# Kernel optimization log

Hardware: AMD Instinct MI355X
Metric: run time of the kernel (lower is better)

## Reference

```python
import jax, jax.numpy as jnp
import numpy as np

M_GRAPHS = 16384
L_FRAGS = 64
L_NODES = 512
N_FOCAL = 3 * M_GRAPHS
N_NEXT = 4 * M_GRAPHS
N_PARTIAL = 262144
D = 64  # Z_dim = EGNN_layer_dim = fragment_library_dim = MLP hidden dim


def _mlp(x, W1, b1, W2, b2):
    # EGNN_MLP: Linear -> LeakyReLU(0.01) -> Linear
    return jnp.dot(jax.nn.leaky_relu(jnp.dot(x, W1) + b1), W2) + b2


def _segment_softmax(scores, seg, num_segments):
    m = jax.ops.segment_max(scores, seg, num_segments=num_segments)
    e = jnp.exp(scores - m[seg])
    s = jax.ops.segment_sum(e, seg, num_segments=num_segments)
    return e / s[seg]


def setup_inputs() -> dict:
    key = jax.random.key(0)
    ks = jax.random.split(key, 32)
    f32 = jnp.float32
    inp = {
        'fragment_library_features': jax.random.normal(ks[0], (L_FRAGS, D), f32),
        'fragment_library_node_features': jax.random.normal(ks[1], (L_NODES, D), f32),
        'graph_subgraph_focal_features_concat': jax.random.normal(ks[2], (M_GRAPHS, D), f32),
        'h_partial': jax.random.normal(ks[3], (N_PARTIAL, D), f32),
        'h_focal': jax.random.normal(ks[4], (N_FOCAL, D), f32),
        'next_atom_type_library_idx': jax.random.randint(ks[5], (M_GRAPHS,), 0, L_FRAGS),
        'stop_mask': jnp.ones((M_GRAPHS,), jnp.bool_),
        'stop_focal_mask': jnp.ones((N_FOCAL,), jnp.bool_),
        'masked_focal_batch_index_reindexed': jnp.arange(N_FOCAL) % M_GRAPHS,
        'focal_attachment_index_rel_partial': jax.random.randint(ks[6], (M_GRAPHS,), 0, N_PARTIAL),
        'next_atom_attachment_indices': jax.random.randint(ks[7], (N_NEXT,), 0, L_NODES),
        'masked_next_atom_attachment_batch_index_reindexed': jnp.arange(N_NEXT) % M_GRAPHS,
        'masked_multihot_next_attachments': jnp.ones((N_NEXT,), jnp.bool_),
    }
    def lin(k, din, dout):
        return jax.random.normal(k, (din, dout), f32) * (1.0 / np.sqrt(din))
    dims = {'stop': (D, 1), 'fatt': (2 * D, 1), 'nfrag': (3 * D, 1), 'nfatt': (4 * D, 1), 'bond': (4 * D, 4)}
    i = 8
    for name, (din, dout) in dims.items():
        inp[name + '_W1'] = lin(ks[i], din, D)
        inp[name + '_b1'] = jax.random.normal(ks[i + 1], (D,), f32) * 0.01
        inp[name + '_W2'] = lin(ks[i + 2], D, dout)
        inp[name + '_b2'] = jax.random.normal(ks[i + 3], (dout,), f32) * 0.01
        i += 4
    return inp


def _forward(flf, flnf, gsf, h_partial, h_focal,
             next_atom_type_library_idx, stop_idx, focal_idx,
             masked_focal_seg, focal_att_idx_rel_partial,
             next_atom_att_idx, next_att_seg, mh_idx,
             stop_W1, stop_b1, stop_W2, stop_b2,
             fatt_W1, fatt_b1, fatt_W2, fatt_b2,
             nfrag_W1, nfrag_b1, nfrag_W2, nfrag_b2,
             nfatt_W1, nfatt_b1, nfatt_W2, nfatt_b2,
             bond_W1, bond_b1, bond_W2, bond_b2):
    # stop scores over all (graph, subgraph, focal) rows
    stop_logits = _mlp(gsf, stop_W1, stop_b1, stop_W2, stop_b2)  # [B, 1]

    h_focal_masked = h_focal[focal_idx]                          # [Nf, D]
    gsf_masked = gsf[stop_idx]                                   # [M, D]
    M = gsf_masked.shape[0]

    # focal attachment scoring: gather graph feats per focal candidate, concat, MLP, segment softmax
    x_fatt = jnp.concatenate([gsf_masked[masked_focal_seg], h_focal_masked], axis=1)  # [Nf, 2D]
    fatt_scores = _mlp(x_fatt, fatt_W1, fatt_b1, fatt_W2, fatt_b2)[:, 0]
    fatt_softmax = _segment_softmax(fatt_scores, masked_focal_seg, M)                 # [Nf]

    # focal atom features gathered from partial-graph node embeddings
    focal_atom_feats = h_partial[focal_att_idx_rel_partial[stop_idx]]                 # [M, D]
    g_focalAtom = jnp.concatenate([gsf_masked, focal_atom_feats], axis=1)             # [M, 2D]

    # cross-product scoring vs fragment library; concat-then-linear == split matmul (no [M,L,3D] materialization)
    din = g_focalAtom.shape[1]
    hA = jnp.dot(g_focalAtom, nfrag_W1[:din])                                         # [M, H]
    hB = jnp.dot(flf, nfrag_W1[din:])                                                 # [L, H]
    hidden = jax.nn.leaky_relu(hA[:, None, :] + hB[None, :, :] + nfrag_b1)            # [M, L, H]
    next_atom_fragment_logits = (jnp.einsum('mlh,ho->mlo', hidden, nfrag_W2) + nfrag_b2)[:, :, 0]  # [M, L]

    # chosen next-fragment features
    next_frag_feats = flf[next_atom_type_library_idx[stop_idx]]                       # [M, D]
    g_nextFrag = jnp.concatenate([g_focalAtom, next_frag_feats], axis=1)              # [M, 3D]

    # next-fragment attachment scoring over candidate library nodes
    next_att_feats = flnf[next_atom_att_idx]                                          # [Nn, D]
    x_nfatt = jnp.concatenate([g_nextFrag[next_att_seg], next_att_feats], axis=1)     # [Nn, 4D]
    nfatt_scores = _mlp(x_nfatt, nfatt_W1, nfatt_b1, nfatt_W2, nfatt_b2)[:, 0]
    nfatt_softmax = _segment_softmax(nfatt_scores, next_att_seg, M)                   # [Nn]

    # bond typing: scatter_mean of equivalent next-atom features per graph
    eq_feats = flnf[next_atom_att_idx[mh_idx]]                                        # [Ne, D]
    seg_mh = next_att_seg[mh_idx]
    sums = jax.ops.segment_sum(eq_feats, seg_mh, num_segments=M)
    cnt = jax.ops.segment_sum(jnp.ones(seg_mh.shape[0], eq_feats.dtype), seg_mh, num_segments=M)
    pooled = sums / jnp.maximum(cnt, 1.0)[:, None]                                    # [M, D]
    g_bond = jnp.concatenate([g_nextFrag, pooled], axis=1)                            # [M, 4D]
    bond_types_logits = _mlp(g_bond, bond_W1, bond_b1, bond_W2, bond_b2)              # [M, 4]

    return (stop_logits, next_atom_fragment_logits, fatt_softmax, nfatt_softmax, bond_types_logits)


def reference(fragment_library_features, fragment_library_node_features,
              graph_subgraph_focal_features_concat, h_partial, h_focal,
              next_atom_type_library_idx, stop_mask, stop_focal_mask,
              masked_focal_batch_index_reindexed, focal_attachment_index_rel_partial,
              next_atom_attachment_indices, masked_next_atom_attachment_batch_index_reindexed,
              masked_multihot_next_attachments,
              stop_W1, stop_b1, stop_W2, stop_b2,
              fatt_W1, fatt_b1, fatt_W2, fatt_b2,
              nfrag_W1, nfrag_b1, nfrag_W2, nfrag_b2,
              nfatt_W1, nfatt_b1, nfatt_W2, nfatt_b2,
              bond_W1, bond_b1, bond_W2, bond_b2):
    # masks are concrete -> convert boolean masks to static index arrays
    stop_idx = np.nonzero(np.asarray(stop_mask))[0]
    focal_idx = np.nonzero(np.asarray(stop_focal_mask))[0]
    mh_idx = np.nonzero(np.asarray(masked_multihot_next_attachments))[0]
    return _forward(fragment_library_features, fragment_library_node_features,
                    graph_subgraph_focal_features_concat, h_partial, h_focal,
                    next_atom_type_library_idx, stop_idx, focal_idx,
                    masked_focal_batch_index_reindexed, focal_attachment_index_rel_partial,
                    next_atom_attachment_indices, masked_next_atom_attachment_batch_index_reindexed,
                    mh_idx,
                    stop_W1, stop_b1, stop_W2, stop_b2,
                    fatt_W1, fatt_b1, fatt_W2, fatt_b2,
                    nfrag_W1, nfrag_b1, nfrag_W2, nfrag_b2,
                    nfatt_W1, nfatt_b1, nfatt_W2, nfatt_b2,
                    bond_W1, bond_b1, bond_W2, bond_b2)
```

## Files before the change

### kernel.cpp

```cpp
#include <hip/hip_runtime.h>
#include <math.h>

#define MG 16384
#define NFOC (3 * MG)
#define NNXT (4 * MG)

typedef float f32x4 __attribute__((ext_vector_type(4)));
typedef short s16x8 __attribute__((ext_vector_type(8)));

#define WT_STOP 0
#define WT_FATT 4096
#define WT_NFRAG 12288
#define WT_NFATT 20480
#define WT_BOND 36864
#define WT_TOTAL 53248

#define SW(r, b) ((b) ^ (((r) & 7) << 4))


__device__ __forceinline__ float lrelu(float x) { return x > 0.f ? x : 0.01f * x; }

__device__ __forceinline__ unsigned short f2bf(float f) {
  union { float f; unsigned u; } a;
  a.f = f;
  unsigned u = a.u;
  unsigned r = (u + 0x7fffu + ((u >> 16) & 1u)) >> 16;
  return (unsigned short)r;
}

__global__ void prep(const float* __restrict__ flf,
                     const float* __restrict__ stopW1,
                     const float* __restrict__ fattW1,
                     const float* __restrict__ nfragW1,
                     const float* __restrict__ nfattW1,
                     const float* __restrict__ bondW1,
                     float* __restrict__ hB4, unsigned short* __restrict__ wt) {
  int b = blockIdx.x, t = threadIdx.x;
  if (b < 16) {
    int l = b * 4 + (t >> 6), h = t & 63;
    float acc = 0.f;
#pragma unroll 8
    for (int k = 0; k < 64; ++k)
      acc = fmaf(flf[l * 64 + k], nfragW1[(128 + k) * 64 + h], acc);
    hB4[(h >> 2) * 256 + l * 4 + (h & 3)] = acc;
  } else {
    int e = (b - 16) * 256 + t;
    if (e < WT_TOTAL) {
      int k_all = e >> 6, col = e & 63;
      const float* src;
      int k, base;
      if (k_all < 64) { src = stopW1; k = k_all; base = WT_STOP; }
      else if (k_all < 192) { src = fattW1; k = k_all - 64; base = WT_FATT; }
      else if (k_all < 320) { src = nfragW1; k = k_all - 192; base = WT_NFRAG; }
      else if (k_all < 576) { src = nfattW1; k = k_all - 320; base = WT_NFATT; }
      else { src = bondW1; k = k_all - 576; base = WT_BOND; }
      int kt = k >> 5, kg = (k >> 3) & 3, ki = k & 7;
      wt[base + (((kt * 4 + kg) * 64 + col) << 3) + ki] = f2bf(src[k * 64 + col]);
    }
  }
}

__device__ __forceinline__ float4 stage_row(char* tileBase, int r, int c4,
                                            const float* srcRow) {
  float4 v = *((const float4*)srcRow + c4);
  unsigned long long pk =
      (unsigned long long)f2bf(v.x) | ((unsigned long long)f2bf(v.y) << 16) |
      ((unsigned long long)f2bf(v.z) << 32) | ((unsigned long long)f2bf(v.w) << 48);
  *(unsigned long long*)(tileBase + r * 128 + SW(r, c4 * 8)) = pk;
  return v;
}

__device__ __forceinline__ s16x8 ldA(const char* tile, int ktLocal, int lane) {
  int r = lane & 15, kg = lane >> 4;
  int b = ktLocal * 64 + kg * 16;
  return *(const s16x8*)(tile + r * 128 + SW(r, b));
}

__device__ __forceinline__ s16x8 ldB(const unsigned short* wt, int base,
                                     int ktGlobal, int kg, int col) {
  return *(const s16x8*)(wt + base + (((ktGlobal * 4 + kg) * 64 + col) << 3));
}

__global__ __launch_bounds__(256, 8) void decoder_main(
    const float* __restrict__ flf, const float* __restrict__ flnf,
    const float* __restrict__ gsf, const float* __restrict__ hpart,
    const float* __restrict__ hfoc,
    const int* __restrict__ nidx, const int* __restrict__ faidx,
    const int* __restrict__ naidx,
    const float* __restrict__ stopB1, const float* __restrict__ stopW2,
    const float* __restrict__ stopB2,
    const float* __restrict__ fattB1, const float* __restrict__ fattW2,
    const float* __restrict__ fattB2,
    const float* __restrict__ nfragB1, const float* __restrict__ nfragW2,
    const float* __restrict__ nfragB2,
    const float* __restrict__ nfattB1, const float* __restrict__ nfattW2,
    const float* __restrict__ nfattB2,
    const float* __restrict__ bondB1, const float* __restrict__ bondW2,
    const float* __restrict__ bondB2,
    const float* __restrict__ hB4, const unsigned short* __restrict__ wt,
    float* __restrict__ out) {
  const int tid = threadIdx.x;
  const int lane = tid & 63;
  const int w = tid >> 6;
  const int kg = lane >> 4;
  const int cl = lane & 15;
  const int col = w * 16 + cl;
  const int bid = (int)blockIdx.x;
  const int type = bid >> 10;
  const int m0 = (bid & 1023) * 16;

  float* o_stop = out;
  float* o_nfrag = out + MG;
  float* o_fatt = out + MG + MG * 64;
  float* o_nfatt = o_fatt + NFOC;
  float* o_bond = o_nfatt + NNXT;

  __shared__ char tiles[14336];
  __shared__ float hAl[16][68];
  __shared__ float scp[4][4][16];
  char* TG = tiles;
  char* TP = tiles + 2048;
  char* T2 = tiles + 4096;
  char* T3 = tiles + 6144;

  {
    int r = tid >> 4, c4 = tid & 15;
    int m = m0 + r;
    stage_row(TG, r, c4, gsf + (size_t)m * 64);
    stage_row(TP, r, c4, hpart + (size_t)faidx[m] * 64);
    if (type == 0) {
#pragma unroll
      for (int rr = 0; rr < 3; ++rr)
        stage_row(T2 + rr * 2048, r, c4, hfoc + (size_t)(m + rr * MG) * 64);
    } else if (type == 1) {
      stage_row(T2, r, c4, flf + (size_t)nidx[m] * 64);
#pragma unroll
      for (int rr = 0; rr < 4; ++rr)
        stage_row(T3 + rr * 2048, r, c4, flnf + (size_t)naidx[m + rr * MG] * 64);
    } else {
      stage_row(T2, r, c4, flf + (size_t)nidx[m] * 64);
      float px = 0.f, py = 0.f, pz = 0.f, pw = 0.f;
#pragma unroll
      for (int rr = 0; rr < 4; ++rr) {
        float4 v = *((const float4*)(flnf + (size_t)naidx[m + rr * MG] * 64) + c4);
        px += v.x; py += v.y; pz += v.z; pw += v.w;
      }
      unsigned long long pk = (unsigned long long)f2bf(0.25f * px) |
                              ((unsigned long long)f2bf(0.25f * py) << 16) |
                              ((unsigned long long)f2bf(0.25f * pz) << 32) |
                              ((unsigned long long)f2bf(0.25f * pw) << 48);
      *(unsigned long long*)(T3 + r * 128 + SW(r, c4 * 8)) = pk;
    }
  }
  __syncthreads();

#define MFMA(a, b, c) __builtin_amdgcn_mfma_f32_16x16x32_bf16(a, b, c, 0, 0, 0)
#define RED16(p, slot)                                                     \
  {                                                                        \
    _Pragma("unroll") for (int off = 1; off < 16; off <<= 1) {             \
      p[0] += __shfl_xor(p[0], off); p[1] += __shfl_xor(p[1], off);        \
      p[2] += __shfl_xor(p[2], off); p[3] += __shfl_xor(p[3], off);        \
    }                                                                      \
    if (cl == 0) {                                                         \
      float* d = &scp[w][slot][kg * 4];                                    \
      d[0] = p[0]; d[1] = p[1]; d[2] = p[2]; d[3] = p[3];                  \
    }                                                                      \
  }

  if (type == 0) {
    {
      float b1 = stopB1[col];
      f32x4 acc = {b1, b1, b1, b1};
      acc = MFMA(ldA(TG, 0, lane), ldB(wt, WT_STOP, 0, kg, col), acc);
      acc = MFMA(ldA(TG, 1, lane), ldB(wt, WT_STOP, 1, kg, col), acc);
      float w2 = stopW2[col];
      f32x4 p;
#pragma unroll
      for (int i = 0; i < 4; ++i) p[i] = lrelu(acc[i]) * w2;
      RED16(p, 0);
    }
    {
      float b1 = fattB1[col];
      f32x4 aS = {b1, b1, b1, b1};
      aS = MFMA(ldA(TG, 0, lane), ldB(wt, WT_FATT, 0, kg, col), aS);
      aS = MFMA(ldA(TG, 1, lane), ldB(wt, WT_FATT, 1, kg, col), aS);
      float w2 = fattW2[col];
#pragma unroll
      for (int rr = 0; rr < 3; ++rr) {
        f32x4 acc = aS;
        acc = MFMA(ldA(T2 + rr * 2048, 0, lane), ldB(wt, WT_FATT, 2, kg, col), acc);
        acc = MFMA(ldA(T2 + rr * 2048, 1, lane), ldB(wt, WT_FATT, 3, kg, col), acc);
        f32x4 p;
#pragma unroll
        for (int i = 0; i < 4; ++i) p[i] = lrelu(acc[i]) * w2;
        RED16(p, 1 + rr);
      }
    }
    {
      float b1 = nfragB1[col];
      f32x4 acc = {b1, b1, b1, b1};
      acc = MFMA(ldA(TG, 0, lane), ldB(wt, WT_NFRAG, 0, kg, col), acc);
      acc = MFMA(ldA(TG, 1, lane), ldB(wt, WT_NFRAG, 1, kg, col), acc);
      acc = MFMA(ldA(TP, 0, lane), ldB(wt, WT_NFRAG, 2, kg, col), acc);
      acc = MFMA(ldA(TP, 1, lane), ldB(wt, WT_NFRAG, 3, kg, col), acc);
#pragma unroll
      for (int i = 0; i < 4; ++i) hAl[kg * 4 + i][col] = acc[i];
    }
    __syncthreads();
    {
      float accL[4] = {0.f, 0.f, 0.f, 0.f};
#pragma unroll
      for (int hg = 0; hg < 16; ++hg) {
        f32x4 hb = *(const f32x4*)(hB4 + hg * 256 + lane * 4);
        f32x4 w2v = *(const f32x4*)(nfragW2 + hg * 4);
#pragma unroll
        for (int mi = 0; mi < 4; ++mi) {
          f32x4 ha = *(const f32x4*)(&hAl[w * 4 + mi][hg * 4]);
#pragma unroll
          for (int j = 0; j < 4; ++j) {
            float x = ha[j] + hb[j];
            accL[mi] = fmaf(fmaxf(x, 0.01f * x), w2v[j], accL[mi]);
          }
        }
      }
#pragma unroll
      for (int mi = 0; mi < 4; ++mi)
        o_nfrag[(size_t)(m0 + w * 4 + mi) * 64 + lane] = accL[mi] + nfragB2[0];
    }
    if (tid < 32) {
      int mm = tid & 15;
      int m = m0 + mm;
      if (tid < 16) {
        float s = scp[0][0][mm] + scp[1][0][mm] + scp[2][0][mm] + scp[3][0][mm];
        o_stop[m] = s + stopB2[0];
      } else {
        float sc[3];
#pragma unroll
        for (int r = 0; r < 3; ++r)
          sc[r] = scp[0][1 + r][mm] + scp[1][1 + r][mm] + scp[2][1 + r][mm] +
                  scp[3][1 + r][mm] + fattB2[0];
        float mx = fmaxf(fmaxf(sc[0], sc[1]), sc[2]);
        float e0 = expf(sc[0] - mx), e1 = expf(sc[1] - mx), e2 = expf(sc[2] - mx);
        float inv = 1.f / (e0 + e1 + e2);
        o_fatt[m] = e0 * inv;
        o_fatt[m + MG] = e1 * inv;
        o_fatt[m + 2 * MG] = e2 * inv;
      }
    }
  } else if (type == 1) {
    {
      float b1 = nfattB1[col];
      f32x4 aS = {b1, b1, b1, b1};
      aS = MFMA(ldA(TG, 0, lane), ldB(wt, WT_NFATT, 0, kg, col), aS);
      aS = MFMA(ldA(TG, 1, lane), ldB(wt, WT_NFATT, 1, kg, col), aS);
      aS = MFMA(ldA(TP, 0, lane), ldB(wt, WT_NFATT, 2, kg, col), aS);
      aS = MFMA(ldA(TP, 1, lane), ldB(wt, WT_NFATT, 3, kg, col), aS);
      aS = MFMA(ldA(T2, 0, lane), ldB(wt, WT_NFATT, 4, kg, col), aS);
      aS = MFMA(ldA(T2, 1, lane), ldB(wt, WT_NFATT, 5, kg, col), aS);
      float w2 = nfattW2[col];
#pragma unroll
      for (int rr = 0; rr < 4; ++rr) {
        f32x4 acc = aS;
        acc = MFMA(ldA(T3 + rr * 2048, 0, lane), ldB(wt, WT_NFATT, 6, kg, col), acc);
        acc = MFMA(ldA(T3 + rr * 2048, 1, lane), ldB(wt, WT_NFATT, 7, kg, col), acc);
        f32x4 p;
#pragma unroll
        for (int i = 0; i < 4; ++i) p[i] = lrelu(acc[i]) * w2;
        RED16(p, rr);
      }
    }
    __syncthreads();
    if (tid < 16) {
      int m = m0 + tid;
      float sc[4];
#pragma unroll
      for (int r = 0; r < 4; ++r)
        sc[r] = scp[0][r][tid] + scp[1][r][tid] + scp[2][r][tid] +
                scp[3][r][tid] + nfattB2[0];
      float mx = fmaxf(fmaxf(sc[0], sc[1]), fmaxf(sc[2], sc[3]));
      float e0 = expf(sc[0] - mx), e1 = expf(sc[1] - mx), e2 = expf(sc[2] - mx),
            e3 = expf(sc[3] - mx);
      float inv = 1.f / (e0 + e1 + e2 + e3);
      o_nfatt[m] = e0 * inv;
      o_nfatt[m + MG] = e1 * inv;
      o_nfatt[m + 2 * MG] = e2 * inv;
      o_nfatt[m + 3 * MG] = e3 * inv;
    }
  } else {
    {
      float b1 = bondB1[col];
      f32x4 acc = {b1, b1, b1, b1};
      acc = MFMA(ldA(TG, 0, lane), ldB(wt, WT_BOND, 0, kg, col), acc);
      acc = MFMA(ldA(TG, 1, lane), ldB(wt, WT_BOND, 1, kg, col), acc);
      acc = MFMA(ldA(TP, 0, lane), ldB(wt, WT_BOND, 2, kg, col), acc);
      acc = MFMA(ldA(TP, 1, lane), ldB(wt, WT_BOND, 3, kg, col), acc);
      acc = MFMA(ldA(T2, 0, lane), ldB(wt, WT_BOND, 4, kg, col), acc);
      acc = MFMA(ldA(T2, 1, lane), ldB(wt, WT_BOND, 5, kg, col), acc);
      acc = MFMA(ldA(T3, 0, lane), ldB(wt, WT_BOND, 6, kg, col), acc);
      acc = MFMA(ldA(T3, 1, lane), ldB(wt, WT_BOND, 7, kg, col), acc);
#pragma unroll
      for (int o = 0; o < 4; ++o) {
        float w2 = bondW2[col * 4 + o];
        f32x4 p;
#pragma unroll
        for (int i = 0; i < 4; ++i) p[i] = lrelu(acc[i]) * w2;
        RED16(p, o);
      }
    }
    __syncthreads();
    if (tid < 16) {
      int m = m0 + tid;
#pragma unroll
      for (int o = 0; o < 4; ++o) {
        float s = scp[0][o][tid] + scp[1][o][tid] + scp[2][o][tid] +
                  scp[3][o][tid];
        o_bond[m * 4 + o] = s + bondB2[o];
      }
    }
  }
}

extern "C" void kernel_launch(void* const* d_in, const int* in_sizes, int n_in,
                              void* d_out, int out_size, void* d_ws, size_t ws_size,
                              hipStream_t stream) {
  const float* flf = (const float*)d_in[0];
  const float* flnf = (const float*)d_in[1];
  const float* gsf = (const float*)d_in[2];
  const float* hpart = (const float*)d_in[3];
  const float* hfoc = (const float*)d_in[4];
  const int* nidx = (const int*)d_in[5];
  const int* faidx = (const int*)d_in[9];
  const int* naidx = (const int*)d_in[10];

  const float* stopW1 = (const float*)d_in[13];
  const float* stopB1 = (const float*)d_in[14];
  const float* stopW2 = (const float*)d_in[15];
  const float* stopB2 = (const float*)d_in[16];
  const float* fattW1 = (const float*)d_in[17];
  const float* fattB1 = (const float*)d_in[18];
  const float* fattW2 = (const float*)d_in[19];
  const float* fattB2 = (const float*)d_in[20];
  const float* nfragW1 = (const float*)d_in[21];
  const float* nfragB1 = (const float*)d_in[22];
  const float* nfragW2 = (const float*)d_in[23];
  const float* nfragB2 = (const float*)d_in[24];
  const float* nfattW1 = (const float*)d_in[25];
  const float* nfattB1 = (const float*)d_in[26];
  const float* nfattW2 = (const float*)d_in[27];
  const float* nfattB2 = (const float*)d_in[28];
  const float* bondW1 = (const float*)d_in[29];
  const float* bondB1 = (const float*)d_in[30];
  const float* bondW2 = (const float*)d_in[31];
  const float* bondB2 = (const float*)d_in[32];

  float* hB4 = (float*)d_ws;
  unsigned short* wtb = (unsigned short*)((char*)d_ws + 16384);

  prep<<<16 + (WT_TOTAL + 255) / 256, 256, 0, stream>>>(
      flf, stopW1, fattW1, nfragW1, nfattW1, bondW1, hB4, wtb);

  decoder_main<<<3 * 1024, 256, 0, stream>>>(
      flf, flnf, gsf, hpart, hfoc, nidx, faidx, naidx,
      stopB1, stopW2, stopB2,
      fattB1, fattW2, fattB2,
      nfragB1, nfragW2, nfragB2,
      nfattB1, nfattW2, nfattB2,
      bondB1, bondW2, bondB2,
      hB4, wtb, (float*)d_out);
}
```

Measured before the change: 28.32 us.

## Split nfrag head into its own block type and transpose MFMA operands for cheaper reductions

Moves the nfrag pairwise MLP out of the type-0 blocks into a separate fourth block type, which raises the grid from 3 to 4 block groups and balances work across blocks. Types are now interleaved by block id (bid & 3) instead of contiguous ranges. MFMA operands are swapped so each lane holds four hidden units of one row. The second-layer dot product then needs only two cross-lane shuffles instead of a 16-lane butterfly on four values. h_partial staging is skipped for type 0, which does not use it. This adds more blocks and repeated staging of the graph features in exchange.

```diff
diff --git a/kernel.cpp b/kernel.cpp
--- a/kernel.cpp
+++ b/kernel.cpp
@@ -105,9 +105,10 @@
   const int kg = lane >> 4;
   const int cl = lane & 15;
   const int col = w * 16 + cl;
+  const int hb = w * 16 + kg * 4;
   const int bid = (int)blockIdx.x;
-  const int type = bid >> 10;
-  const int m0 = (bid & 1023) * 16;
+  const int type = bid & 3;
+  const int m0 = (bid >> 2) * 16;
 
   float* o_stop = out;
   float* o_nfrag = out + MG;
@@ -127,17 +128,18 @@
     int r = tid >> 4, c4 = tid & 15;
     int m = m0 + r;
     stage_row(TG, r, c4, gsf + (size_t)m * 64);
-    stage_row(TP, r, c4, hpart + (size_t)faidx[m] * 64);
     if (type == 0) {
 #pragma unroll
       for (int rr = 0; rr < 3; ++rr)
         stage_row(T2 + rr * 2048, r, c4, hfoc + (size_t)(m + rr * MG) * 64);
     } else if (type == 1) {
+      stage_row(TP, r, c4, hpart + (size_t)faidx[m] * 64);
       stage_row(T2, r, c4, flf + (size_t)nidx[m] * 64);
 #pragma unroll
       for (int rr = 0; rr < 4; ++rr)
         stage_row(T3 + rr * 2048, r, c4, flnf + (size_t)naidx[m + rr * MG] * 64);
-    } else {
+    } else if (type == 2) {
+      stage_row(TP, r, c4, hpart + (size_t)faidx[m] * 64);
       stage_row(T2, r, c4, flf + (size_t)nidx[m] * 64);
       float px = 0.f, py = 0.f, pz = 0.f, pw = 0.f;
 #pragma unroll
@@ -150,83 +152,48 @@
                               ((unsigned long long)f2bf(0.25f * pz) << 32) |
                               ((unsigned long long)f2bf(0.25f * pw) << 48);
       *(unsigned long long*)(T3 + r * 128 + SW(r, c4 * 8)) = pk;
+    } else {
+      stage_row(TP, r, c4, hpart + (size_t)faidx[m] * 64);
     }
   }
   __syncthreads();
 
 #define MFMA(a, b, c) __builtin_amdgcn_mfma_f32_16x16x32_bf16(a, b, c, 0, 0, 0)
-#define RED16(p, slot)                                                     \
+#define REDT(v, slot)                                                      \
   {                                                                        \
-    _Pragma("unroll") for (int off = 1; off < 16; off <<= 1) {             \
-      p[0] += __shfl_xor(p[0], off); p[1] += __shfl_xor(p[1], off);        \
-      p[2] += __shfl_xor(p[2], off); p[3] += __shfl_xor(p[3], off);        \
-    }                                                                      \
-    if (cl == 0) {                                                         \
-      float* d = &scp[w][slot][kg * 4];                                    \
-      d[0] = p[0]; d[1] = p[1]; d[2] = p[2]; d[3] = p[3];                  \
-    }                                                                      \
+    v += __shfl_xor(v, 16);                                                \
+    v += __shfl_xor(v, 32);                                                \
+    if (lane < 16) scp[w][slot][lane] = v;                                 \
   }
 
   if (type == 0) {
     {
-      float b1 = stopB1[col];
-      f32x4 acc = {b1, b1, b1, b1};
-      acc = MFMA(ldA(TG, 0, lane), ldB(wt, WT_STOP, 0, kg, col), acc);
-      acc = MFMA(ldA(TG, 1, lane), ldB(wt, WT_STOP, 1, kg, col), acc);
-      float w2 = stopW2[col];
-      f32x4 p;
-#pragma unroll
-      for (int i = 0; i < 4; ++i) p[i] = lrelu(acc[i]) * w2;
-      RED16(p, 0);
-    }
-    {
-      float b1 = fattB1[col];
-      f32x4 aS = {b1, b1, b1, b1};
-      aS = MFMA(ldA(TG, 0, lane), ldB(wt, WT_FATT, 0, kg, col), aS);
-      aS = MFMA(ldA(TG, 1, lane), ldB(wt, WT_FATT, 1, kg, col), aS);
-      float w2 = fattW2[col];
+      f32x4 acc = *(const f32x4*)(stopB1 + hb);
+      acc = MFMA(ldB(wt, WT_STOP, 0, kg, col), ldA(TG, 0, lane), acc);
+      acc = MFMA(ldB(wt, WT_STOP, 1, kg, col), ldA(TG, 1, lane), acc);
+      f32x4 w2 = *(const f32x4*)(stopW2 + hb);
+      float v = 0.f;
+#pragma unroll
+      for (int i = 0; i < 4; ++i) v = fmaf(lrelu(acc[i]), w2[i], v);
+      REDT(v, 0);
+    }
+    {
+      f32x4 aS = *(const f32x4*)(fattB1 + hb);
+      aS = MFMA(ldB(wt, WT_FATT, 0, kg, col), ldA(TG, 0, lane), aS);
+      aS = MFMA(ldB(wt, WT_FATT, 1, kg, col), ldA(TG, 1, lane), aS);
+      f32x4 w2 = *(const f32x4*)(fattW2 + hb);
 #pragma unroll
       for (int rr = 0; rr < 3; ++rr) {
         f32x4 acc = aS;
-        acc = MFMA(ldA(T2 + rr * 2048, 0, lane), ldB(wt, WT_FATT, 2, kg, col), acc);
-        acc = MFMA(ldA(T2 + rr * 2048, 1, lane), ldB(wt, WT_FATT, 3, kg, col), acc);
-        f32x4 p;
-#pragma unroll
-        for (int i = 0; i < 4; ++i) p[i] = lrelu(acc[i]) * w2;
-        RED16(p, 1 + rr);
-      }
-    }
-    {
-      float b1 = nfragB1[col];
-      f32x4 acc = {b1, b1, b1, b1};
-      acc = MFMA(ldA(TG, 0, lane), ldB(wt, WT_NFRAG, 0, kg, col), acc);
-      acc = MFMA(ldA(TG, 1, lane), ldB(wt, WT_NFRAG, 1, kg, col), acc);
-      acc = MFMA(ldA(TP, 0, lane), ldB(wt, WT_NFRAG, 2, kg, col), acc);
-      acc = MFMA(ldA(TP, 1, lane), ldB(wt, WT_NFRAG, 3, kg, col), acc);
-#pragma unroll
-      for (int i = 0; i < 4; ++i) hAl[kg * 4 + i][col] = acc[i];
+        acc = MFMA(ldB(wt, WT_FATT, 2, kg, col), ldA(T2 + rr * 2048, 0, lane), acc);
+        acc = MFMA(ldB(wt, WT_FATT, 3, kg, col), ldA(T2 + rr * 2048, 1, lane), acc);
+        float v = 0.f;
+#pragma unroll
+        for (int i = 0; i < 4; ++i) v = fmaf(lrelu(acc[i]), w2[i], v);
+        REDT(v, 1 + rr);
+      }
     }
     __syncthreads();
-    {
-      float accL[4] = {0.f, 0.f, 0.f, 0.f};
-#pragma unroll
-      for (int hg = 0; hg < 16; ++hg) {
-        f32x4 hb = *(const f32x4*)(hB4 + hg * 256 + lane * 4);
-        f32x4 w2v = *(const f32x4*)(nfragW2 + hg * 4);
-#pragma unroll
-        for (int mi = 0; mi < 4; ++mi) {
-          f32x4 ha = *(const f32x4*)(&hAl[w * 4 + mi][hg * 4]);
-#pragma unroll
-          for (int j = 0; j < 4; ++j) {
-            float x = ha[j] + hb[j];
-            accL[mi] = fmaf(fmaxf(x, 0.01f * x), w2v[j], accL[mi]);
-          }
-        }
-      }
-#pragma unroll
-      for (int mi = 0; mi < 4; ++mi)
-        o_nfrag[(size_t)(m0 + w * 4 + mi) * 64 + lane] = accL[mi] + nfragB2[0];
-    }
     if (tid < 32) {
       int mm = tid & 15;
       int m = m0 + mm;
@@ -249,24 +216,23 @@
     }
   } else if (type == 1) {
     {
-      float b1 = nfattB1[col];
-      f32x4 aS = {b1, b1, b1, b1};
-      aS = MFMA(ldA(TG, 0, lane), ldB(wt, WT_NFATT, 0, kg, col), aS);
-      aS = MFMA(ldA(TG, 1, lane), ldB(wt, WT_NFATT, 1, kg, col), aS);
-      aS = MFMA(ldA(TP, 0, lane), ldB(wt, WT_NFATT, 2, kg, col), aS);
-      aS = MFMA(ldA(TP, 1, lane), ldB(wt, WT_NFATT, 3, kg, col), aS);
-      aS = MFMA(ldA(T2, 0, lane), ldB(wt, WT_NFATT, 4, kg, col), aS);
-      aS = MFMA(ldA(T2, 1, lane), ldB(wt, WT_NFATT, 5, kg, col), aS);
-      float w2 = nfattW2[col];
+      f32x4 aS = *(const f32x4*)(nfattB1 + hb);
+      aS = MFMA(ldB(wt, WT_NFATT, 0, kg, col), ldA(TG, 0, lane), aS);
+      aS = MFMA(ldB(wt, WT_NFATT, 1, kg, col), ldA(TG, 1, lane), aS);
+      aS = MFMA(ldB(wt, WT_NFATT, 2, kg, col), ldA(TP, 0, lane), aS);
+      aS = MFMA(ldB(wt, WT_NFATT, 3, kg, col), ldA(TP, 1, lane), aS);
+      aS = MFMA(ldB(wt, WT_NFATT, 4, kg, col), ldA(T2, 0, lane), aS);
+      aS = MFMA(ldB(wt, WT_NFATT, 5, kg, col), ldA(T2, 1, lane), aS);
+      f32x4 w2 = *(const f32x4*)(nfattW2 + hb);
 #pragma unroll
       for (int rr = 0; rr < 4; ++rr) {
         f32x4 acc = aS;
-        acc = MFMA(ldA(T3 + rr * 2048, 0, lane), ldB(wt, WT_NFATT, 6, kg, col), acc);
-        acc = MFMA(ldA(T3 + rr * 2048, 1, lane), ldB(wt, WT_NFATT, 7, kg, col), acc);
-        f32x4 p;
-#pragma unroll
-        for (int i = 0; i < 4; ++i) p[i] = lrelu(acc[i]) * w2;
-        RED16(p, rr);
+        acc = MFMA(ldB(wt, WT_NFATT, 6, kg, col), ldA(T3 + rr * 2048, 0, lane), acc);
+        acc = MFMA(ldB(wt, WT_NFATT, 7, kg, col), ldA(T3 + rr * 2048, 1, lane), acc);
+        float v = 0.f;
+#pragma unroll
+        for (int i = 0; i < 4; ++i) v = fmaf(lrelu(acc[i]), w2[i], v);
+        REDT(v, rr);
       }
     }
     __syncthreads();
@@ -286,25 +252,30 @@
       o_nfatt[m + 2 * MG] = e2 * inv;
       o_nfatt[m + 3 * MG] = e3 * inv;
     }
-  } else {
-    {
-      float b1 = bondB1[col];
-      f32x4 acc = {b1, b1, b1, b1};
-      acc = MFMA(ldA(TG, 0, lane), ldB(wt, WT_BOND, 0, kg, col), acc);
-      acc = MFMA(ldA(TG, 1, lane), ldB(wt, WT_BOND, 1, kg, col), acc);
-      acc = MFMA(ldA(TP, 0, lane), ldB(wt, WT_BOND, 2, kg, col), acc);
-      acc = MFMA(ldA(TP, 1, lane), ldB(wt, WT_BOND, 3, kg, col), acc);
-      acc = MFMA(ldA(T2, 0, lane), ldB(wt, WT_BOND, 4, kg, col), acc);
-      acc = MFMA(ldA(T2, 1, lane), ldB(wt, WT_BOND, 5, kg, col), acc);
-      acc = MFMA(ldA(T3, 0, lane), ldB(wt, WT_BOND, 6, kg, col), acc);
-      acc = MFMA(ldA(T3, 1, lane), ldB(wt, WT_BOND, 7, kg, col), acc);
+  } else if (type == 2) {
+    {
+      f32x4 acc = *(const f32x4*)(bondB1 + hb);
+      acc = MFMA(ldB(wt, WT_BOND, 0, kg, col), ldA(TG, 0, lane), acc);
+      acc = MFMA(ldB(wt, WT_BOND, 1, kg, col), ldA(TG, 1, lane), acc);
+      acc = MFMA(ldB(wt, WT_BOND, 2, kg, col), ldA(TP, 0, lane), acc);
+      acc = MFMA(ldB(wt, WT_BOND, 3, kg, col), ldA(TP, 1, lane), acc);
+      acc = MFMA(ldB(wt, WT_BOND, 4, kg, col), ldA(T2, 0, lane), acc);
+      acc = MFMA(ldB(wt, WT_BOND, 5, kg, col), ldA(T2, 1, lane), acc);
+      acc = MFMA(ldB(wt, WT_BOND, 6, kg, col), ldA(T3, 0, lane), acc);
+      acc = MFMA(ldB(wt, WT_BOND, 7, kg, col), ldA(T3, 1, lane), acc);
+      float l4[4];
+      f32x4 bw[4];
+#pragma unroll
+      for (int i = 0; i < 4; ++i) {
+        l4[i] = lrelu(acc[i]);
+        bw[i] = *(const f32x4*)(bondW2 + (hb + i) * 4);
+      }
 #pragma unroll
       for (int o = 0; o < 4; ++o) {
-        float w2 = bondW2[col * 4 + o];
-        f32x4 p;
-#pragma unroll
-        for (int i = 0; i < 4; ++i) p[i] = lrelu(acc[i]) * w2;
-        RED16(p, o);
+        float v = 0.f;
+#pragma unroll
+        for (int i = 0; i < 4; ++i) v = fmaf(l4[i], bw[i][o], v);
+        REDT(v, o);
       }
     }
     __syncthreads();
@@ -316,6 +287,38 @@
                   scp[3][o][tid];
         o_bond[m * 4 + o] = s + bondB2[o];
       }
+    }
+  } else {
+    {
+      float b1 = nfragB1[col];
+      f32x4 acc = {b1, b1, b1, b1};
+      acc = MFMA(ldA(TG, 0, lane), ldB(wt, WT_NFRAG, 0, kg, col), acc);
+      acc = MFMA(ldA(TG, 1, lane), ldB(wt, WT_NFRAG, 1, kg, col), acc);
+      acc = MFMA(ldA(TP, 0, lane), ldB(wt, WT_NFRAG, 2, kg, col), acc);
+      acc = MFMA(ldA(TP, 1, lane), ldB(wt, WT_NFRAG, 3, kg, col), acc);
+#pragma unroll
+      for (int i = 0; i < 4; ++i) hAl[kg * 4 + i][col] = acc[i];
+    }
+    __syncthreads();
+    {
+      float accL[4] = {0.f, 0.f, 0.f, 0.f};
+#pragma unroll
+      for (int hg = 0; hg < 16; ++hg) {
+        f32x4 hb4v = *(const f32x4*)(hB4 + hg * 256 + lane * 4);
+        f32x4 w2v = *(const f32x4*)(nfragW2 + hg * 4);
+#pragma unroll
+        for (int mi = 0; mi < 4; ++mi) {
+          f32x4 ha = *(const f32x4*)(&hAl[w * 4 + mi][hg * 4]);
+#pragma unroll
+          for (int j = 0; j < 4; ++j) {
+            float x = ha[j] + hb4v[j];
+            accL[mi] = fmaf(fmaxf(x, 0.01f * x), w2v[j], accL[mi]);
+          }
+        }
+      }
+#pragma unroll
+      for (int mi = 0; mi < 4; ++mi)
+        o_nfrag[(size_t)(m0 + w * 4 + mi) * 64 + lane] = accL[mi] + nfragB2[0];
     }
   }
 }
@@ -359,7 +362,7 @@
   prep<<<16 + (WT_TOTAL + 255) / 256, 256, 0, stream>>>(
       flf, stopW1, fattW1, nfragW1, nfattW1, bondW1, hB4, wtb);
 
-  decoder_main<<<3 * 1024, 256, 0, stream>>>(
+  decoder_main<<<4 * 1024, 256, 0, stream>>>(
       flf, flnf, gsf, hpart, hfoc, nidx, faidx, naidx,
       stopB1, stopW2, stopB2,
       fattB1, fattW2, fattB2,
```

After: 36.53 us. 29.0% more time.
